# Kernel optimization log

Hardware: AMD Instinct MI355X
Metric: run time of the kernel (lower is better)

The kernel has to match this reference:

```python
import jax, jax.numpy as jnp
import numpy as np

B, NPG, K, HID, MAXZ = 512, 256, 60, 128, 1000
NTOT = B * NPG            # 131072 nodes
DEG = 16
E = NTOT * DEG            # 2097152 edges
TLD = HID * 3 + 1         # 385 = total_latent_dim
DENSE = (K // 2 - 5 + 1) * 32  # 832


def setup_inputs() -> dict:
    key = jax.random.key(0)
    ks = jax.random.split(key, 20)
    # within-graph random edges, offset per graph
    loc = jax.random.randint(ks[0], (2, B, NPG * DEG), 0, NPG)
    offs = (jnp.arange(B) * NPG)[None, :, None]
    edge_index = (loc + offs).reshape(2, E).astype(jnp.int32)
    z = jax.random.randint(ks[1], (NTOT,), 0, MAXZ).astype(jnp.int32)
    edge_weight = jax.random.uniform(ks[2], (E,), dtype=jnp.float32)
    z_table = jax.random.normal(ks[3], (MAXZ, HID), dtype=jnp.float32) * 0.1
    W0 = jax.random.normal(ks[4], (HID, HID)) * 0.05
    W1 = jax.random.normal(ks[5], (HID, HID)) * 0.05
    W2 = jax.random.normal(ks[6], (HID, HID)) * 0.05
    W3 = jax.random.normal(ks[7], (HID, 1)) * 0.05
    b0 = jnp.zeros((HID,)); b1 = jnp.zeros((HID,)); b2 = jnp.zeros((HID,)); b3 = jnp.zeros((1,))
    conv1_w = jax.random.normal(ks[8], (16, 1, TLD)) * 0.05
    conv1_b = jnp.zeros((16,))
    conv2_w = jax.random.normal(ks[9], (32, 16, 5)) * 0.05
    conv2_b = jnp.zeros((32,))
    lin1_w = jax.random.normal(ks[10], (DENSE, 128)) * 0.05
    lin1_b = jnp.zeros((128,))
    lin2_w = jax.random.normal(ks[11], (128, 1)) * 0.05
    lin2_b = jnp.zeros((1,))
    return {"z_table": z_table, "W0": W0, "b0": b0, "W1": W1, "b1": b1,
            "W2": W2, "b2": b2, "W3": W3, "b3": b3,
            "conv1_w": conv1_w, "conv1_b": conv1_b, "conv2_w": conv2_w, "conv2_b": conv2_b,
            "lin1_w": lin1_w, "lin1_b": lin1_b, "lin2_w": lin2_w, "lin2_b": lin2_b,
            "edge_weight": edge_weight, "z": z, "edge_index": edge_index}


def reference(z_table, W0, b0, W1, b1, W2, b2, W3, b3,
              conv1_w, conv1_b, conv2_w, conv2_b,
              lin1_w, lin1_b, lin2_w, lin2_b,
              edge_weight, z, edge_index):
    # --- GCN normalization with self loops (symmetric) ---
    loops = jnp.arange(NTOT, dtype=edge_index.dtype)
    src = jnp.concatenate([edge_index[0], loops])
    dst = jnp.concatenate([edge_index[1], loops])
    ew = jnp.concatenate([edge_weight, jnp.ones((NTOT,), edge_weight.dtype)])
    deg = jax.ops.segment_sum(ew, dst, num_segments=NTOT)
    dinv = jnp.where(deg > 0, jax.lax.rsqrt(jnp.maximum(deg, 1e-12)), 0.0)
    norm = dinv[src] * ew * dinv[dst]

    def gcn(x, W, b):
        h = x @ W
        agg = jax.ops.segment_sum(h[src] * norm[:, None], dst, num_segments=NTOT)
        return agg + b

    x = z_table[z]                              # [NTOT, HID]
    xs = []
    for (W, b) in ((W0, b0), (W1, b1), (W2, b2), (W3, b3)):
        x = jnp.tanh(gcn(x, W, b))
        xs.append(x)
    x = jnp.concatenate(xs, axis=-1)            # [NTOT, 385]

    # --- global sort pool (descending by last channel, top-k per graph) ---
    xg = x.reshape(B, NPG, TLD)
    idx = jnp.argsort(-xg[:, :, -1], axis=1)[:, :K]
    pooled = jnp.take_along_axis(xg, idx[:, :, None], axis=1)   # [B, K, 385]
    y = pooled.reshape(B, 1, K * TLD)

    # --- dense conv1d / MLP head ---
    y = jax.lax.conv_general_dilated(y, conv1_w, (TLD,), 'VALID',
                                     dimension_numbers=('NCH', 'OIH', 'NCH'))
    y = jax.nn.relu(y + conv1_b[None, :, None])                  # [B,16,K]
    y = y.reshape(B, 16, K // 2, 2).max(axis=-1)                 # maxpool(2,2)
    y = jax.lax.conv_general_dilated(y, conv2_w, (1,), 'VALID',
                                     dimension_numbers=('NCH', 'OIH', 'NCH'))
    y = jax.nn.relu(y + conv2_b[None, :, None])                  # [B,32,26]
    y = y.reshape(B, -1)                                         # [B,832]
    y = jax.nn.relu(y @ lin1_w + lin1_b)
    return y @ lin2_w + lin2_b                                   # [B,1]
```

## Files before the change

kernel.cpp:

```cpp
#include <hip/hip_runtime.h>
#include <math.h>

#define NTOT   131072
#define NPG    256
#define BGR    512
#define HID    128
#define EDG    2097152
#define EPG    4096
#define EPGP   4864
#define KTOP   60
#define TLDIM  385

__device__ __forceinline__ int physX(int row, int c4) {
    return (c4 + row + (row >> 3)) & 31;
}
__device__ __forceinline__ int physA(int row, int c4) {
    return (c4 + (row >> 3) + ((row & 1) << 2)) & 31;
}

__global__ __launch_bounds__(1024, 4) void k_gnn(
        const float* __restrict__ zt, const int* __restrict__ z,
        const int* __restrict__ ei, const float* __restrict__ ew,
        const float* __restrict__ W0, const float* __restrict__ b0,
        const float* __restrict__ W1, const float* __restrict__ b1,
        const float* __restrict__ W2, const float* __restrict__ b2,
        const float* __restrict__ W3, const float* __restrict__ b3,
        float* __restrict__ X0, float* __restrict__ X1,
        float* __restrict__ P2, float* __restrict__ selK, int* __restrict__ selI) {
    __shared__ float4 XS[NPG * 32];
    __shared__ __align__(16) float wnL[EPGP];
    __shared__ __align__(4) unsigned char esrcL[EPGP];
    __shared__ unsigned short offL[NPG + 2];
    __shared__ unsigned short mLn[NPG];
    __shared__ int    cntL[NPG];
    __shared__ float  selfnL[NPG];
    __shared__ float  dinvL[NPG];
    __shared__ float  t3s[NPG];
    __shared__ float  keyL[NPG];
    __shared__ int    selN[KTOP];

    int t = threadIdx.x;
    int g = blockIdx.x;

    float*          ewL  = (float*)XS;
    unsigned char*  srcB = (unsigned char*)XS + 16384;
    unsigned char*  dstB = (unsigned char*)XS + 20480;
    unsigned int*   hh   = (unsigned int*)((char*)XS + 24576);

    for (int j = t; j < EPG; j += 1024) {
        int e = g * EPG + j;
        ewL[j]  = ew[e];
        srcB[j] = (unsigned char)(ei[e] & (NPG - 1));
        dstB[j] = (unsigned char)(ei[EDG + e] & (NPG - 1));
    }
    for (int i = t; i < 64 * 257; i += 1024) hh[i] = 0;
    __syncthreads();
    if (t < 64) {
        int base = t * 64;
        unsigned int* hr = hh + t * 257;
        for (int i = 0; i < 64; i++) hr[dstB[base + i]]++;
    }
    __syncthreads();
    if (t < NPG) {
        int tot = 0;
        for (int c = 0; c < 64; c++) tot += hh[c * 257 + t];
        mLn[t]  = (unsigned short)tot;
        cntL[t] = (tot + 3) & ~3;
    }
    __syncthreads();
    if (t < 64) {
        int carry = 0;
        if (t == 0) offL[0] = 0;
        for (int seg = 0; seg < 4; seg++) {
            int v = cntL[seg * 64 + t];
#pragma unroll
            for (int d = 1; d < 64; d <<= 1) {
                int u = __shfl_up(v, d);
                if (t >= d) v += u;
            }
            offL[seg * 64 + t + 1] = (unsigned short)(v + carry);
            carry += __shfl(v, 63);
        }
    }
    __syncthreads();
    if (t < NPG) {
        int run = offL[t];
        for (int c = 0; c < 64; c++) {
            int tmp = hh[c * 257 + t];
            hh[c * 257 + t] = (unsigned int)run;
            run += tmp;
        }
    }
    __syncthreads();
    if (t < 64) {
        int base = t * 64;
        unsigned int* hr = hh + t * 257;
        for (int i = 0; i < 64; i++) {
            int e = base + i;
            int d = dstB[e];
            int slot = hr[d];
            hr[d] = slot + 1;
            esrcL[slot] = srcB[e];
            wnL[slot]   = ewL[e];
        }
    }
    __syncthreads();
    if (t < NPG) {
        int o = offL[t], m = mLn[t];
        float s = 0.f;
        for (int i = 0; i < m; i++) s += wnL[o + i];
        float dv = 1.0f / sqrtf(s + 1.0f);
        dinvL[t]  = dv;
        selfnL[t] = dv * dv;
    }
    __syncthreads();
    if (t < NPG) {
        int o = offL[t], m = mLn[t], pc = cntL[t];
        float dn = dinvL[t];
        for (int i = 0; i < m; i++)
            wnL[o + i] = dinvL[esrcL[o + i]] * wnL[o + i] * dn;
        for (int i = m; i < pc; i++) {
            esrcL[o + i] = (unsigned char)t;
            wnL[o + i]   = 0.f;
        }
    }
    __syncthreads();
    for (int i = t; i < NPG * 32; i += 1024) {
        int row = i >> 5, c4 = i & 31;
        int zi = z[g * NPG + row];
        XS[row * 32 + physX(row, c4)] = ((const float4*)zt)[(size_t)zi * 32 + c4];
    }
    __syncthreads();

    const unsigned int* esrcW = (const unsigned int*)esrcL;
    const float4*       wn4   = (const float4*)wnL;
    int wid  = t >> 6;
    int l    = t & 63;
    int half = l >> 5;
    int c4   = l & 31;
    int rg  = t & 31;
    int cgq = t >> 5;

#pragma unroll 1
    for (int layer = 0; layer < 3; layer++) {
        const float* W    = (layer == 0) ? W0 : (layer == 1) ? W1 : W2;
        const float* bias = (layer == 0) ? b0 : (layer == 1) ? b1 : b2;
        float* Xout       = (layer == 0) ? X0 : (layer == 1) ? X1 : nullptr;

        float4 accA[8];
#pragma unroll 1
        for (int it = 0; it < 8; it++) {
            int p    = wid * 8 + it;
            int node = 2 * p + half;
            int oA = offL[2 * p], oM = offL[2 * p + 1], oE = offL[2 * p + 2];
            int m4A = (oM - oA) >> 2, m4B = (oE - oM) >> 2;
            int mmax4 = m4A > m4B ? m4A : m4B;
            int o4 = (half ? oM : oA) >> 2;
            int m4 = half ? m4B : m4A;
            unsigned int selfpack = (unsigned int)node * 0x01010101u;
            float4 acc = make_float4(0.f, 0.f, 0.f, 0.f);

            unsigned int s_cur = selfpack, s_nxt = selfpack;
            float4 w_cur = make_float4(0.f, 0.f, 0.f, 0.f);
            float4 w_nxt = make_float4(0.f, 0.f, 0.f, 0.f);
            float4 v0, v1, v2, v3;
            if (mmax4 > 0) {
                {
                    int idx = o4;
                    unsigned int ss = esrcW[idx]; float4 ww = wn4[idx];
                    if (0 >= m4) { ss = selfpack; ww = make_float4(0.f,0.f,0.f,0.f); }
                    s_cur = ss; w_cur = ww;
                }
                {
                    int jc = (1 < m4) ? 1 : (m4 > 0 ? m4 - 1 : 0);
                    int idx = o4 + jc;
                    unsigned int ss = esrcW[idx]; float4 ww = wn4[idx];
                    if (1 >= m4) { ss = selfpack; ww = make_float4(0.f,0.f,0.f,0.f); }
                    s_nxt = ss; w_nxt = ww;
                }
                int a0 =  s_cur        & 255, a1 = (s_cur >> 8)  & 255;
                int a2i = (s_cur >> 16) & 255, a3 = (s_cur >> 24) & 255;
                v0 = XS[a0 * 32 + physX(a0, c4)];
                v1 = XS[a1 * 32 + physX(a1, c4)];
                v2 = XS[a2i * 32 + physX(a2i, c4)];
                v3 = XS[a3 * 32 + physX(a3, c4)];
            }
            for (int j4 = 0; j4 < mmax4; j4++) {
                int b0i =  s_nxt        & 255, b1i = (s_nxt >> 8)  & 255;
                int b2i = (s_nxt >> 16) & 255, b3i = (s_nxt >> 24) & 255;
                float4 n0 = XS[b0i * 32 + physX(b0i, c4)];
                float4 n1 = XS[b1i * 32 + physX(b1i, c4)];
                float4 n2 = XS[b2i * 32 + physX(b2i, c4)];
                float4 n3 = XS[b3i * 32 + physX(b3i, c4)];
                int jn = j4 + 2;
                int jc = (jn < m4) ? jn : (m4 > 0 ? m4 - 1 : 0);
                int idx = o4 + jc;
                unsigned int s2_ = esrcW[idx];
                float4 w2_ = wn4[idx];
                if (jn >= m4) { s2_ = selfpack; w2_ = make_float4(0.f,0.f,0.f,0.f); }
                acc.x += w_cur.x * v0.x; acc.y += w_cur.x * v0.y;
                acc.z += w_cur.x * v0.z; acc.w += w_cur.x * v0.w;
                acc.x += w_cur.y * v1.x; acc.y += w_cur.y * v1.y;
                acc.z += w_cur.y * v1.z; acc.w += w_cur.y * v1.w;
                acc.x += w_cur.z * v2.x; acc.y += w_cur.z * v2.y;
                acc.z += w_cur.z * v2.z; acc.w += w_cur.z * v2.w;
                acc.x += w_cur.w * v3.x; acc.y += w_cur.w * v3.y;
                acc.z += w_cur.w * v3.z; acc.w += w_cur.w * v3.w;
                v0 = n0; v1 = n1; v2 = n2; v3 = n3;
                w_cur = w_nxt; s_nxt = s2_; w_nxt = w2_;
            }
            float wsf = selfnL[node];
            float4 sv = XS[node * 32 + physX(node, c4)];
            acc.x += wsf * sv.x; acc.y += wsf * sv.y;
            acc.z += wsf * sv.z; acc.w += wsf * sv.w;
            accA[it] = acc;
        }
        __syncthreads();
#pragma unroll
        for (int it = 0; it < 8; it++) {
            int node = 2 * (wid * 8 + it) + half;
            XS[node * 32 + physA(node, c4)] = accA[it];
        }
        __syncthreads();

        float a2[8][4];
#pragma unroll
        for (int i = 0; i < 8; i++)
#pragma unroll
            for (int j = 0; j < 4; j++) a2[i][j] = 0.f;
        for (int k4 = 0; k4 < 32; k4++) {
            float4 a4[8];
#pragma unroll
            for (int i = 0; i < 8; i++) {
                int rl = rg * 8 + i;
                a4[i] = XS[rl * 32 + physA(rl, k4)];
            }
            float4 wv[4];
#pragma unroll
            for (int kw = 0; kw < 4; kw++)
                wv[kw] = *(((const float4*)(W + (size_t)(k4 * 4 + kw) * HID)) + cgq);
#pragma unroll
            for (int kw = 0; kw < 4; kw++) {
#pragma unroll
                for (int i = 0; i < 8; i++) {
                    float a = (kw == 0) ? a4[i].x : (kw == 1) ? a4[i].y
                            : (kw == 2) ? a4[i].z : a4[i].w;
                    a2[i][0] += a * wv[kw].x; a2[i][1] += a * wv[kw].y;
                    a2[i][2] += a * wv[kw].z; a2[i][3] += a * wv[kw].w;
                }
            }
        }
        float4 bv = ((const float4*)bias)[cgq];
        float4 oo[8];
#pragma unroll
        for (int i = 0; i < 8; i++) {
            oo[i].x = tanhf(a2[i][0] + bv.x); oo[i].y = tanhf(a2[i][1] + bv.y);
            oo[i].z = tanhf(a2[i][2] + bv.z); oo[i].w = tanhf(a2[i][3] + bv.w);
        }
        __syncthreads();
#pragma unroll
        for (int i = 0; i < 8; i++) {
            int rl = rg * 8 + i;
            XS[rl * 32 + physX(rl, cgq)] = oo[i];
        }
        __syncthreads();
        if (Xout) {
            float4* dst = (float4*)Xout + (size_t)g * NPG * 32;
            for (int i = t; i < NPG * 32; i += 1024) {
                int row = i >> 5, cc = i & 31;
                dst[i] = XS[row * 32 + physX(row, cc)];
            }
        }
    }

    {
        int n = t >> 2, part = t & 3;
        const float4* w4 = (const float4*)W3;
        const float4* rb = XS + n * 32;
        float s = 0.f;
#pragma unroll
        for (int q = 0; q < 8; q++) {
            float4 v = rb[physX(n, part * 8 + q)];
            float4 ww = w4[part * 8 + q];
            s += v.x * ww.x + v.y * ww.y + v.z * ww.z + v.w * ww.w;
        }
        s += __shfl_down(s, 2, 4);
        s += __shfl_down(s, 1, 4);
        if (part == 0) t3s[n] = s;
    }
    __syncthreads();

    if (t < NPG) {
        int o = offL[t], m2 = mLn[t];
        float s = 0.f;
        for (int i = 0; i < m2; i++)
            s += wnL[o + i] * t3s[esrcL[o + i]];
        s += selfnL[t] * t3s[t];
        keyL[t] = tanhf(s + b3[0]);
    }
    __syncthreads();
    if (t < NPG) {
        float ki = keyL[t];
        int rank = 0;
        for (int j = 0; j < NPG; j++) {
            float kj = keyL[j];
            rank += (kj > ki) || (kj == ki && j < t);
        }
        if (rank < KTOP) selN[rank] = t;
    }
    __syncthreads();
    if (t < KTOP) {
        int nd = selN[t];
        selI[g * KTOP + t] = nd;
        selK[g * KTOP + t] = keyL[nd];
    }
    for (int i = t; i < KTOP * 32; i += 1024) {
        int r = i >> 5, q = i & 31;
        int nd = selN[r];
        ((float4*)P2)[(size_t)g * KTOP * 32 + i] = XS[nd * 32 + physX(nd, q)];
    }
}

__global__ __launch_bounds__(256) void k_head(const float* __restrict__ X0,
                                              const float* __restrict__ X1,
                                              const float* __restrict__ P2,
                                              const float* __restrict__ selK,
                                              const int* __restrict__ selI,
                                              const float* __restrict__ c1w,
                                              const float* __restrict__ c1b,
                                              const float* __restrict__ c2w,
                                              const float* __restrict__ c2b,
                                              const float* __restrict__ l1w,
                                              const float* __restrict__ l1b,
                                              const float* __restrict__ l2w,
                                              const float* __restrict__ l2b,
                                              float* __restrict__ out) {
    __shared__ __align__(16) float pch[KTOP * 132];
    __shared__ __align__(16) float w1s[16 * 132];
    __shared__ int   seln[KTOP];
    __shared__ float selk[KTOP];
    __shared__ float c1s[16 * KTOP];
    __shared__ float mps[16 * 30];
    __shared__ float w2s[32 * 80];
    __shared__ float yb[832];
    __shared__ float l1p[256];
    __shared__ float l1v[128];

    int g = blockIdx.x, t = threadIdx.x;
    if (t < KTOP) {
        seln[t] = selI[g * KTOP + t];
        selk[t] = selK[g * KTOP + t];
    }

    float acc1[4] = {0.f, 0.f, 0.f, 0.f};
    for (int tc = 0; tc < 3; tc++) {
        const float* Xsrc = (tc == 0) ? X0 : X1;
        __syncthreads();
        for (int i = t; i < KTOP * 32; i += 256) {
            int k = i >> 5, q = i & 31;
            float4 v;
            if (tc < 2) {
                int nd = seln[k];
                v = ((const float4*)Xsrc)[((size_t)g * NPG + nd) * 32 + q];
            } else {
                v = ((const float4*)P2)[(size_t)g * KTOP * 32 + i];
            }
            *((float4*)&pch[k * 132 + q * 4]) = v;
        }
        for (int i = t; i < 16 * 128; i += 256) {
            int ch = i >> 7, tt = i & 127;
            w1s[ch * 132 + tt] = c1w[ch * TLDIM + tc * 128 + tt];
        }
        __syncthreads();
#pragma unroll
        for (int it = 0; it < 4; it++) {
            int e = it * 256 + t;
            if (e < 960) {
                int k = e >> 4, ch = e & 15;
                const float* pr = &pch[k * 132];
                const float* wr = &w1s[ch * 132];
                float s = 0.f;
#pragma unroll
                for (int q = 0; q < 32; q++) {
                    float4 pv = *((float4*)&pr[q * 4]);
                    float4 wv = *((float4*)&wr[q * 4]);
                    s += pv.x * wv.x + pv.y * wv.y + pv.z * wv.z + pv.w * wv.w;
                }
                acc1[it] += s;
            }
        }
    }
    __syncthreads();
#pragma unroll
    for (int it = 0; it < 4; it++) {
        int e = it * 256 + t;
        if (e < 960) {
            int k = e >> 4, ch = e & 15;
            float v = acc1[it] + selk[k] * c1w[ch * TLDIM + 384] + c1b[ch];
            c1s[ch * KTOP + k] = fmaxf(v, 0.f);
        }
    }
    for (int i = t; i < 2560; i += 256) w2s[i] = c2w[i];
    __syncthreads();
    for (int i = t; i < 480; i += 256) {
        int ch = i / 30, p = i - ch * 30;
        mps[ch * 30 + p] = fmaxf(c1s[ch * KTOP + 2 * p], c1s[ch * KTOP + 2 * p + 1]);
    }
    __syncthreads();
    for (int e = t; e < 832; e += 256) {
        int oc = e / 26, q = e - oc * 26;
        float s = 0.f;
#pragma unroll
        for (int ic = 0; ic < 16; ic++) {
            const float* mr = &mps[ic * 30 + q];
            const float* wr = &w2s[oc * 80 + ic * 5];
#pragma unroll
            for (int j = 0; j < 5; j++) s += mr[j] * wr[j];
        }
        yb[e] = fmaxf(s + c2b[oc], 0.f);
    }
    __syncthreads();
    {
        int u = t & 127, h = t >> 7;
        float s = 0.f;
        for (int d = h * 416; d < h * 416 + 416; d++) s += yb[d] * l1w[d * 128 + u];
        l1p[t] = s;
    }
    __syncthreads();
    if (t < 128) {
        float v = fmaxf(l1p[t] + l1p[t + 128] + l1b[t], 0.f);
        l1v[t] = v * l2w[t];
    }
    __syncthreads();
    if (t < 64) {
        float v = l1v[t] + l1v[t + 64];
        v += __shfl_down(v, 32);
        v += __shfl_down(v, 16);
        v += __shfl_down(v, 8);
        v += __shfl_down(v, 4);
        v += __shfl_down(v, 2);
        v += __shfl_down(v, 1);
        if (t == 0) out[g] = v + l2b[0];
    }
}

extern "C" void kernel_launch(void* const* d_in, const int* in_sizes, int n_in,
                              void* d_out, int out_size, void* d_ws, size_t ws_size,
                              hipStream_t stream) {
    (void)in_sizes; (void)n_in; (void)out_size; (void)ws_size;
    const float* zt  = (const float*)d_in[0];
    const float* W0  = (const float*)d_in[1];
    const float* b0  = (const float*)d_in[2];
    const float* W1  = (const float*)d_in[3];
    const float* b1  = (const float*)d_in[4];
    const float* W2  = (const float*)d_in[5];
    const float* b2  = (const float*)d_in[6];
    const float* W3  = (const float*)d_in[7];
    const float* b3  = (const float*)d_in[8];
    const float* c1w = (const float*)d_in[9];
    const float* c1b = (const float*)d_in[10];
    const float* c2w = (const float*)d_in[11];
    const float* c2b = (const float*)d_in[12];
    const float* l1w = (const float*)d_in[13];
    const float* l1b = (const float*)d_in[14];
    const float* l2w = (const float*)d_in[15];
    const float* l2b = (const float*)d_in[16];
    const float* ew  = (const float*)d_in[17];
    const int*   z   = (const int*)d_in[18];
    const int*   ei  = (const int*)d_in[19];
    float* out = (float*)d_out;

    char* wsp = (char*)d_ws;
    size_t off = 0;
    auto alloc = [&](size_t bytes) -> void* {
        void* p = wsp + off;
        off += (bytes + 255) & ~(size_t)255;
        return p;
    };
    float* X0   = (float*)alloc((size_t)NTOT * HID * 4);
    float* X1   = (float*)alloc((size_t)NTOT * HID * 4);
    float* P2   = (float*)alloc((size_t)BGR * KTOP * HID * 4);
    float* selK = (float*)alloc((size_t)BGR * KTOP * 4);
    int*   selI = (int*)  alloc((size_t)BGR * KTOP * 4);

    k_gnn <<<BGR, dim3(1024), 0, stream>>>(zt, z, ei, ew,
                                           W0, b0, W1, b1, W2, b2, W3, b3,
                                           X0, X1, P2, selK, selI);
    k_head<<<BGR, dim3(256), 0, stream>>>(X0, X1, P2, selK, selI,
                                          c1w, c1b, c2w, c2b,
                                          l1w, l1b, l2w, l2b, out);
}
```

Baseline: 585.7 us.

## Split pooled-row gather into separate kernel and widen head to 512 threads

Moves the top-k gather of layer-0/1 rows out of the head kernel into a new k_pool kernel that writes all three channel blocks into one contiguous packed buffer. The head kernel then reads only that contiguous buffer and runs with 512 threads instead of 256. The gather costs an extra launch and an extra write and read of the pooled data. In exchange the head's loads become contiguous and it has more parallelism.

```diff
diff --git a/kernel.cpp b/kernel.cpp
--- a/kernel.cpp
+++ b/kernel.cpp
@@ -26,7 +26,7 @@
         const float* __restrict__ W2, const float* __restrict__ b2,
         const float* __restrict__ W3, const float* __restrict__ b3,
         float* __restrict__ X0, float* __restrict__ X1,
-        float* __restrict__ P2, float* __restrict__ selK, int* __restrict__ selI) {
+        float* __restrict__ P, float* __restrict__ selK, int* __restrict__ selI) {
     __shared__ float4 XS[NPG * 32];
     __shared__ __align__(16) float wnL[EPGP];
     __shared__ __align__(4) unsigned char esrcL[EPGP];
@@ -317,15 +317,30 @@
     for (int i = t; i < KTOP * 32; i += 1024) {
         int r = i >> 5, q = i & 31;
         int nd = selN[r];
-        ((float4*)P2)[(size_t)g * KTOP * 32 + i] = XS[nd * 32 + physX(nd, q)];
-    }
-}
-
-__global__ __launch_bounds__(256) void k_head(const float* __restrict__ X0,
+        ((float4*)P)[((size_t)(g * 3 + 2)) * (KTOP * 32) + i] = XS[nd * 32 + physX(nd, q)];
+    }
+}
+
+__global__ __launch_bounds__(256) void k_pool(const float* __restrict__ X0,
                                               const float* __restrict__ X1,
-                                              const float* __restrict__ P2,
+                                              const int* __restrict__ selI,
+                                              float* __restrict__ P) {
+    __shared__ int sn[KTOP];
+    int g = blockIdx.x, t = threadIdx.x;
+    if (t < KTOP) sn[t] = selI[g * KTOP + t];
+    __syncthreads();
+    for (int i = t; i < KTOP * 32; i += 256) {
+        int k = i >> 5, q = i & 31;
+        int nd = sn[k];
+        ((float4*)P)[((size_t)(g * 3 + 0)) * (KTOP * 32) + i] =
+            ((const float4*)X0)[((size_t)g * NPG + nd) * 32 + q];
+        ((float4*)P)[((size_t)(g * 3 + 1)) * (KTOP * 32) + i] =
+            ((const float4*)X1)[((size_t)g * NPG + nd) * 32 + q];
+    }
+}
+
+__global__ __launch_bounds__(512) void k_head(const float* __restrict__ P,
                                               const float* __restrict__ selK,
-                                              const int* __restrict__ selI,
                                               const float* __restrict__ c1w,
                                               const float* __restrict__ c1b,
                                               const float* __restrict__ c2w,
@@ -337,7 +352,6 @@
                                               float* __restrict__ out) {
     __shared__ __align__(16) float pch[KTOP * 132];
     __shared__ __align__(16) float w1s[16 * 132];
-    __shared__ int   seln[KTOP];
     __shared__ float selk[KTOP];
     __shared__ float c1s[16 * KTOP];
     __shared__ float mps[16 * 30];
@@ -347,34 +361,24 @@
     __shared__ float l1v[128];
 
     int g = blockIdx.x, t = threadIdx.x;
-    if (t < KTOP) {
-        seln[t] = selI[g * KTOP + t];
-        selk[t] = selK[g * KTOP + t];
-    }
-
-    float acc1[4] = {0.f, 0.f, 0.f, 0.f};
+    if (t < KTOP) selk[t] = selK[g * KTOP + t];
+
+    float acc1[2] = {0.f, 0.f};
     for (int tc = 0; tc < 3; tc++) {
-        const float* Xsrc = (tc == 0) ? X0 : X1;
-        __syncthreads();
-        for (int i = t; i < KTOP * 32; i += 256) {
+        __syncthreads();
+        for (int i = t; i < KTOP * 32; i += 512) {
             int k = i >> 5, q = i & 31;
-            float4 v;
-            if (tc < 2) {
-                int nd = seln[k];
-                v = ((const float4*)Xsrc)[((size_t)g * NPG + nd) * 32 + q];
-            } else {
-                v = ((const float4*)P2)[(size_t)g * KTOP * 32 + i];
-            }
-            *((float4*)&pch[k * 132 + q * 4]) = v;
-        }
-        for (int i = t; i < 16 * 128; i += 256) {
+            *((float4*)&pch[k * 132 + q * 4]) =
+                ((const float4*)P)[((size_t)(g * 3 + tc)) * (KTOP * 32) + i];
+        }
+        for (int i = t; i < 16 * 128; i += 512) {
             int ch = i >> 7, tt = i & 127;
             w1s[ch * 132 + tt] = c1w[ch * TLDIM + tc * 128 + tt];
         }
         __syncthreads();
 #pragma unroll
-        for (int it = 0; it < 4; it++) {
-            int e = it * 256 + t;
+        for (int it = 0; it < 2; it++) {
+            int e = it * 512 + t;
             if (e < 960) {
                 int k = e >> 4, ch = e & 15;
                 const float* pr = &pch[k * 132];
@@ -392,22 +396,22 @@
     }
     __syncthreads();
 #pragma unroll
-    for (int it = 0; it < 4; it++) {
-        int e = it * 256 + t;
+    for (int it = 0; it < 2; it++) {
+        int e = it * 512 + t;
         if (e < 960) {
             int k = e >> 4, ch = e & 15;
             float v = acc1[it] + selk[k] * c1w[ch * TLDIM + 384] + c1b[ch];
             c1s[ch * KTOP + k] = fmaxf(v, 0.f);
         }
     }
-    for (int i = t; i < 2560; i += 256) w2s[i] = c2w[i];
-    __syncthreads();
-    for (int i = t; i < 480; i += 256) {
-        int ch = i / 30, p = i - ch * 30;
+    for (int i = t; i < 2560; i += 512) w2s[i] = c2w[i];
+    __syncthreads();
+    if (t < 480) {
+        int ch = t / 30, p = t - ch * 30;
         mps[ch * 30 + p] = fmaxf(c1s[ch * KTOP + 2 * p], c1s[ch * KTOP + 2 * p + 1]);
     }
     __syncthreads();
-    for (int e = t; e < 832; e += 256) {
+    for (int e = t; e < 832; e += 512) {
         int oc = e / 26, q = e - oc * 26;
         float s = 0.f;
 #pragma unroll
@@ -420,7 +424,7 @@
         yb[e] = fmaxf(s + c2b[oc], 0.f);
     }
     __syncthreads();
-    {
+    if (t < 256) {
         int u = t & 127, h = t >> 7;
         float s = 0.f;
         for (int d = h * 416; d < h * 416 + 416; d++) s += yb[d] * l1w[d * 128 + u];
@@ -479,14 +483,15 @@
     };
     float* X0   = (float*)alloc((size_t)NTOT * HID * 4);
     float* X1   = (float*)alloc((size_t)NTOT * HID * 4);
-    float* P2   = (float*)alloc((size_t)BGR * KTOP * HID * 4);
+    float* P    = (float*)alloc((size_t)BGR * 3 * KTOP * HID * 4);
     float* selK = (float*)alloc((size_t)BGR * KTOP * 4);
     int*   selI = (int*)  alloc((size_t)BGR * KTOP * 4);
 
     k_gnn <<<BGR, dim3(1024), 0, stream>>>(zt, z, ei, ew,
                                            W0, b0, W1, b1, W2, b2, W3, b3,
-                                           X0, X1, P2, selK, selI);
-    k_head<<<BGR, dim3(256), 0, stream>>>(X0, X1, P2, selK, selI,
+                                           X0, X1, P, selK, selI);
+    k_pool<<<BGR, dim3(256), 0, stream>>>(X0, X1, selI, P);
+    k_head<<<BGR, dim3(512), 0, stream>>>(P, selK,
                                           c1w, c1b, c2w, c2b,
                                           l1w, l1b, l2w, l2b, out);
 }
```

New measurement: 590.1 us. About the same (+0.7%).
